# Kernel tuning notes

Measured on AMD Instinct MI355X. Metric: run time of the kernel, lower is better.

The kernel has to match this reference:

```python
import jax, jax.numpy as jnp
import numpy as np

N_NODES = 100000
N_EDGES = 1600000
NUM_GRAPHS = 64
D = 128      # num_node_features
H = 256      # hidden_dim
OUT = 1      # output_dim
GA = 6       # num_graph_attributes


def setup_inputs() -> dict:
    key = jax.random.key(0)
    ks = jax.random.split(key, 20)
    p = lambda k, shape: (jax.random.normal(k, shape, jnp.float32) * 0.02)
    return {
        "x": jax.random.normal(ks[0], (N_NODES, D), jnp.float32),
        "edge_index": jax.random.randint(ks[1], (2, N_EDGES), 0, N_NODES),
        "batch": jnp.sort(jax.random.randint(ks[2], (N_NODES,), 0, NUM_GRAPHS)),
        "graph_attr": jax.random.normal(ks[3], (NUM_GRAPHS, GA), jnp.float32),
        # conv1 MLP: Linear(D->H), ReLU, Linear(H->H)
        "w1a": p(ks[4], (D, H)), "b1a": p(ks[5], (H,)),
        "w1b": p(ks[6], (H, H)), "b1b": p(ks[7], (H,)),
        # conv2 MLP: Linear(H->H), ReLU, Linear(H->H)
        "w2a": p(ks[8], (H, H)), "b2a": p(ks[9], (H,)),
        "w2b": p(ks[10], (H, H)), "b2b": p(ks[11], (H,)),
        # head
        "wf1": p(ks[12], (H + GA, H)), "bf1": p(ks[13], (H,)),
        "wf2": p(ks[14], (H, OUT)), "bf2": p(ks[15], (OUT,)),
    }


def _gin_conv(x, src, dst, wa, ba, wb, bb):
    # GINConv with default eps=0: MLP((1+0)*x_i + sum_{j->i} x_j)
    agg = jax.ops.segment_sum(x[src], dst, num_segments=N_NODES)  # [N, d]
    h = x + agg
    h = jax.nn.relu(h @ wa + ba)
    return h @ wb + bb


def reference(x, edge_index, batch, graph_attr,
              w1a, b1a, w1b, b1b, w2a, b2a, w2b, b2b,
              wf1, bf1, wf2, bf2):
    src, dst = edge_index[0], edge_index[1]
    h = jax.nn.relu(_gin_conv(x, src, dst, w1a, b1a, w1b, b1b))  # [N, H]
    h = _gin_conv(h, src, dst, w2a, b2a, w2b, b2b)               # [N, H]
    # global mean pool per graph
    sums = jax.ops.segment_sum(h, batch, num_segments=NUM_GRAPHS)          # [G, H]
    cnts = jax.ops.segment_sum(jnp.ones((h.shape[0], 1), h.dtype), batch,
                               num_segments=NUM_GRAPHS)                    # [G, 1]
    pooled = sums / jnp.maximum(cnts, 1.0)
    g = jnp.concatenate([pooled, graph_attr.reshape(-1, GA)], axis=1)      # [G, H+GA]
    g = jax.nn.relu(g @ wf1 + bf1)
    return g @ wf2 + bf2                                                   # [G, OUT]
```

## Files before the change

kernel.cpp:

```cpp
#include <hip/hip_runtime.h>

#define N_NODES 100000
#define N_EDGES 1600000
#define NGRAPH  64
#define DIN     128
#define HID     256
#define GA      6

#define NBUCK  196
#define BSHIFT 9
#define BCAP   10240

typedef __attribute__((ext_vector_type(8))) short bf16x8;
typedef __attribute__((ext_vector_type(4))) float f32x4;

__device__ __forceinline__ unsigned short f2bf(float f) {
  unsigned int u = __float_as_uint(f);
  u += 0x7fffu + ((u >> 16) & 1u);
  return (unsigned short)(u >> 16);
}
__device__ __forceinline__ float bf_lo(unsigned int u) { return __uint_as_float(u << 16); }
__device__ __forceinline__ float bf_hi(unsigned int u) { return __uint_as_float(u & 0xffff0000u); }
__device__ __forceinline__ unsigned int packbf(float lo, float hi) {
  return (unsigned int)f2bf(lo) | ((unsigned int)f2bf(hi) << 16);
}

__device__ __forceinline__ void gload16(const void* g, void* l) {
  __builtin_amdgcn_global_load_lds(
      (const __attribute__((address_space(1))) unsigned int*)g,
      (__attribute__((address_space(3))) unsigned int*)l, 16, 0, 0);
}


__global__ __launch_bounds__(256) void cvt_all(const float* __restrict__ x,
                                               const float* __restrict__ w1a,
                                               const float* __restrict__ w1b,
                                               const float* __restrict__ w2a,
                                               const float* __restrict__ w2b,
                                               unsigned short* __restrict__ xo,
                                               unsigned short* __restrict__ o1a,
                                               unsigned short* __restrict__ o1b,
                                               unsigned short* __restrict__ o2a,
                                               unsigned short* __restrict__ o2b) {
  int bid = blockIdx.x, tid = threadIdx.x;
  if (bid < 12500) {
    size_t idx = ((size_t)bid * 256 + tid) * 4;
    float4 v = *(const float4*)&x[idx];
    ushort4 o;
    o.x = f2bf(v.x); o.y = f2bf(v.y); o.z = f2bf(v.z); o.w = f2bf(v.w);
    *(ushort4*)&xo[idx] = o;
    return;
  }
  bid -= 12500;
  const float* in; unsigned short* out; int shift, idx;
  if (bid < 128)      { in = w1a; out = o1a; shift = 7; idx = bid * 256 + tid; }
  else if (bid < 384) { in = w1b; out = o1b; shift = 8; idx = (bid - 128) * 256 + tid; }
  else if (bid < 640) { in = w2a; out = o2a; shift = 8; idx = (bid - 384) * 256 + tid; }
  else                { in = w2b; out = o2b; shift = 8; idx = (bid - 640) * 256 + tid; }
  int K = 1 << shift;
  int n = idx >> shift;
  int k = idx & (K - 1);
  out[idx] = f2bf(in[(size_t)k * HID + n]);
}


__global__ __launch_bounds__(256) void bin_kernel(const int* __restrict__ esrc,
                                                  const int* __restrict__ edst,
                                                  int* __restrict__ cursor,
                                                  unsigned int* __restrict__ tmp) {
  __shared__ unsigned int pk[4096];
  __shared__ unsigned char bkb[4096];
  __shared__ int hist[NBUCK], lbase[NBUCK + 1], gbase[NBUCK], lcur[NBUCK];
  const int tid = threadIdx.x;
  const int lane = tid & 63;
  const int ebase = blockIdx.x * 4096;
  const int n = min(4096, N_EDGES - ebase);
  if (tid < NBUCK) hist[tid] = 0;
  __syncthreads();
  unsigned int pkv[16]; int bk[16];
#pragma unroll
  for (int i = 0; i < 16; i++) {
    int e = ebase + i * 256 + tid;
    bk[i] = -1;
    if (e < N_EDGES) {
      int s = esrc[e], d = edst[e];
      bk[i] = d >> BSHIFT;
      pkv[i] = (unsigned int)s | ((unsigned int)(d & ((1 << BSHIFT) - 1)) << 17);
      atomicAdd(&hist[bk[i]], 1);
    }
  }
  __syncthreads();
  if (tid < 64) {
    int i0 = 4 * tid;
    int a0 = (i0 + 0 < NBUCK) ? hist[i0 + 0] : 0;
    int a1 = (i0 + 1 < NBUCK) ? hist[i0 + 1] : 0;
    int a2 = (i0 + 2 < NBUCK) ? hist[i0 + 2] : 0;
    int a3 = (i0 + 3 < NBUCK) ? hist[i0 + 3] : 0;
    int p = a0 + a1 + a2 + a3, sc = p;
#pragma unroll
    for (int off = 1; off < 64; off <<= 1) {
      int t = __shfl_up(sc, off);
      if (lane >= off) sc += t;
    }
    int excl = sc - p;
    if (i0 + 0 < NBUCK) lbase[i0 + 0] = excl;
    if (i0 + 1 < NBUCK) lbase[i0 + 1] = excl + a0;
    if (i0 + 2 < NBUCK) lbase[i0 + 2] = excl + a0 + a1;
    if (i0 + 3 < NBUCK) lbase[i0 + 3] = excl + a0 + a1 + a2;
    if (tid == 63) lbase[NBUCK] = sc;
  }
  __syncthreads();
  if (tid < NBUCK) {
    int c = hist[tid];
    gbase[tid] = c ? atomicAdd(&cursor[tid], c) : 0;
    lcur[tid] = lbase[tid];
  }
  __syncthreads();
#pragma unroll
  for (int i = 0; i < 16; i++) {
    if (bk[i] >= 0) {
      int pos = atomicAdd(&lcur[bk[i]], 1);
      pk[pos] = pkv[i];
      bkb[pos] = (unsigned char)bk[i];
    }
  }
  __syncthreads();
#pragma unroll
  for (int i = 0; i < 16; i++) {
    int idx = i * 256 + tid;
    if (idx < n) {
      int b = bkb[idx];
      tmp[(size_t)b * BCAP + gbase[b] + (idx - lbase[b])] = pk[idx];
    }
  }
}


__global__ __launch_bounds__(512) void sort_kernel(const unsigned int* __restrict__ tmp,
                                                   const int* __restrict__ cnt,
                                                   int* __restrict__ csr,
                                                   int* __restrict__ ssrc) {
  __shared__ int nhist[512], ncur[512];
  __shared__ int bb[NBUCK];
  __shared__ int wsum[8];
  const int b = blockIdx.x;
  const int tid = threadIdx.x;
  const int lane = tid & 63, wid = tid >> 6;
  if (tid < 64) {
    int i0 = 4 * tid;
    int a0 = (i0 + 0 < NBUCK) ? cnt[i0 + 0] : 0;
    int a1 = (i0 + 1 < NBUCK) ? cnt[i0 + 1] : 0;
    int a2 = (i0 + 2 < NBUCK) ? cnt[i0 + 2] : 0;
    int a3 = (i0 + 3 < NBUCK) ? cnt[i0 + 3] : 0;
    int p = a0 + a1 + a2 + a3, sc = p;
#pragma unroll
    for (int off = 1; off < 64; off <<= 1) {
      int t = __shfl_up(sc, off);
      if (lane >= off) sc += t;
    }
    int excl = sc - p;
    if (i0 + 0 < NBUCK) bb[i0 + 0] = excl;
    if (i0 + 1 < NBUCK) bb[i0 + 1] = excl + a0;
    if (i0 + 2 < NBUCK) bb[i0 + 2] = excl + a0 + a1;
    if (i0 + 3 < NBUCK) bb[i0 + 3] = excl + a0 + a1 + a2;
  }
  nhist[tid] = 0;
  __syncthreads();
  const int myCnt = cnt[b];
  const int ebase = bb[b];
  const unsigned int* srcp = tmp + (size_t)b * BCAP;
  for (int i = tid; i < myCnt; i += 512)
    atomicAdd(&nhist[srcp[i] >> 17], 1);
  __syncthreads();
  int v = nhist[tid];
  int sc = v;
#pragma unroll
  for (int off = 1; off < 64; off <<= 1) {
    int t = __shfl_up(sc, off);
    if (lane >= off) sc += t;
  }
  if (lane == 63) wsum[wid] = sc;
  __syncthreads();
  if (tid < 8) {
    int ws = wsum[tid];
#pragma unroll
    for (int off = 1; off < 8; off <<= 1) {
      int t = __shfl_up(ws, off);
      if (tid >= off) ws += t;
    }
    wsum[tid] = ws;
  }
  __syncthreads();
  int excl = ((wid > 0) ? wsum[wid - 1] : 0) + sc - v;
  ncur[tid] = excl;
  int node0 = (b << BSHIFT) + tid;
  if (node0 < N_NODES) csr[node0] = ebase + excl;
  if (b == 0 && tid == 0) csr[N_NODES] = N_EDGES;
  __syncthreads();
  for (int i = tid; i < myCnt; i += 512) {
    unsigned int pe = srcp[i];
    int pos = atomicAdd(&ncur[pe >> 17], 1);
    ssrc[ebase + pos] = (int)(pe & 0x1FFFF);
  }
}


__global__ __launch_bounds__(256) void agg1_kernel(const uint2* __restrict__ x,
                                                   const int* __restrict__ csr,
                                                   const int* __restrict__ ssrc,
                                                   uint2* __restrict__ out) {
  int node = blockIdx.x * 4 + (threadIdx.x >> 6);
  int lane = threadIdx.x & 63;
  int half = lane >> 5;
  int dl   = lane & 31;
  float a0 = 0.f, a1 = 0.f, a2 = 0.f, a3 = 0.f;
  if (half == 0) {
    uint2 u = x[(size_t)node * 32 + dl];
    a0 = bf_lo(u.x); a1 = bf_hi(u.x); a2 = bf_lo(u.y); a3 = bf_hi(u.y);
  }
  int s = csr[node], e = csr[node + 1];
  int i = s;
  for (; i + 8 <= e; i += 8) {
    int s0 = ssrc[i + half],     s1 = ssrc[i + 2 + half];
    int s2 = ssrc[i + 4 + half], s3 = ssrc[i + 6 + half];
    uint2 v0 = x[(size_t)s0 * 32 + dl];
    uint2 v1 = x[(size_t)s1 * 32 + dl];
    uint2 v2 = x[(size_t)s2 * 32 + dl];
    uint2 v3 = x[(size_t)s3 * 32 + dl];
    a0 += bf_lo(v0.x) + bf_lo(v1.x) + bf_lo(v2.x) + bf_lo(v3.x);
    a1 += bf_hi(v0.x) + bf_hi(v1.x) + bf_hi(v2.x) + bf_hi(v3.x);
    a2 += bf_lo(v0.y) + bf_lo(v1.y) + bf_lo(v2.y) + bf_lo(v3.y);
    a3 += bf_hi(v0.y) + bf_hi(v1.y) + bf_hi(v2.y) + bf_hi(v3.y);
  }
  for (; i + 2 <= e; i += 2) {
    int sn = ssrc[i + half];
    uint2 v = x[(size_t)sn * 32 + dl];
    a0 += bf_lo(v.x); a1 += bf_hi(v.x);
    a2 += bf_lo(v.y); a3 += bf_hi(v.y);
  }
  if (i < e && half == 0) {
    uint2 v = x[(size_t)ssrc[i] * 32 + dl];
    a0 += bf_lo(v.x); a1 += bf_hi(v.x);
    a2 += bf_lo(v.y); a3 += bf_hi(v.y);
  }
  a0 += __shfl_xor(a0, 32);
  a1 += __shfl_xor(a1, 32);
  a2 += __shfl_xor(a2, 32);
  a3 += __shfl_xor(a3, 32);
  if (half == 0) {
    uint2 o;
    o.x = packbf(a0, a1);
    o.y = packbf(a2, a3);
    out[(size_t)node * 32 + dl] = o;
  }
}

__global__ __launch_bounds__(256) void agg2_kernel(const uint2* __restrict__ x,
                                                   const int* __restrict__ csr,
                                                   const int* __restrict__ ssrc,
                                                   uint2* __restrict__ out) {
  int node = blockIdx.x * 4 + (threadIdx.x >> 6);
  int lane = threadIdx.x & 63;
  uint2 u = x[(size_t)node * 64 + lane];
  float a0 = bf_lo(u.x), a1 = bf_hi(u.x), a2 = bf_lo(u.y), a3 = bf_hi(u.y);
  int s = csr[node], e = csr[node + 1];
  int i = s;
  for (; i + 8 <= e; i += 8) {
    int n0 = ssrc[i],     n1 = ssrc[i + 1], n2 = ssrc[i + 2], n3 = ssrc[i + 3];
    int n4 = ssrc[i + 4], n5 = ssrc[i + 5], n6 = ssrc[i + 6], n7 = ssrc[i + 7];
    uint2 v0 = x[(size_t)n0 * 64 + lane];
    uint2 v1 = x[(size_t)n1 * 64 + lane];
    uint2 v2 = x[(size_t)n2 * 64 + lane];
    uint2 v3 = x[(size_t)n3 * 64 + lane];
    uint2 v4 = x[(size_t)n4 * 64 + lane];
    uint2 v5 = x[(size_t)n5 * 64 + lane];
    uint2 v6 = x[(size_t)n6 * 64 + lane];
    uint2 v7 = x[(size_t)n7 * 64 + lane];
    a0 += (bf_lo(v0.x) + bf_lo(v1.x)) + (bf_lo(v2.x) + bf_lo(v3.x)) +
          (bf_lo(v4.x) + bf_lo(v5.x)) + (bf_lo(v6.x) + bf_lo(v7.x));
    a1 += (bf_hi(v0.x) + bf_hi(v1.x)) + (bf_hi(v2.x) + bf_hi(v3.x)) +
          (bf_hi(v4.x) + bf_hi(v5.x)) + (bf_hi(v6.x) + bf_hi(v7.x));
    a2 += (bf_lo(v0.y) + bf_lo(v1.y)) + (bf_lo(v2.y) + bf_lo(v3.y)) +
          (bf_lo(v4.y) + bf_lo(v5.y)) + (bf_lo(v6.y) + bf_lo(v7.y));
    a3 += (bf_hi(v0.y) + bf_hi(v1.y)) + (bf_hi(v2.y) + bf_hi(v3.y)) +
          (bf_hi(v4.y) + bf_hi(v5.y)) + (bf_hi(v6.y) + bf_hi(v7.y));
  }
  for (; i < e; i++) {
    uint2 v = x[(size_t)ssrc[i] * 64 + lane];
    a0 += bf_lo(v.x); a1 += bf_hi(v.x);
    a2 += bf_lo(v.y); a3 += bf_hi(v.y);
  }
  uint2 o;
  o.x = packbf(a0, a1);
  o.y = packbf(a2, a3);
  out[(size_t)node * 64 + lane] = o;
}


template<int K, bool RELU>
__global__ __launch_bounds__(512)
void gemm128(const unsigned short* __restrict__ A,
             const unsigned short* __restrict__ Wt,
             const float* __restrict__ bias,
             unsigned short* __restrict__ C) {
  __shared__ unsigned short Asl[128 * 64];
  __shared__ unsigned short Wsl[256 * 64];
  const int tid = threadIdx.x;
  const int lane = tid & 63;
  const int w = tid >> 6;
  const int wm = w >> 2;
  const int wn = w & 3;
  const int l15 = lane & 15, l4 = lane >> 4, l7 = lane & 7;
  const int rowBase = blockIdx.x * 128;

  f32x4 acc[4][4] = {};

  for (int k0 = 0; k0 < K; k0 += 64) {
#pragma unroll
    for (int i = 0; i < 2; i++) {
      int c = i * 512 + tid;
      int m = c >> 3, koL = c & 7;
      int koS = koL ^ (m & 7);
      int gr = rowBase + m; if (gr >= N_NODES) gr = N_NODES - 1;
      gload16(&A[(size_t)gr * K + k0 + koS * 8], Asl + (size_t)c * 8);
    }
#pragma unroll
    for (int i = 0; i < 4; i++) {
      int c = i * 512 + tid;
      int n = c >> 3, koL = c & 7;
      int koS = koL ^ (n & 7);
      gload16(&Wt[(size_t)n * K + k0 + koS * 8], Wsl + (size_t)c * 8);
    }
    __syncthreads();
#pragma unroll
    for (int kk = 0; kk < 2; kk++) {
      int koX = (kk * 4 + l4) ^ l7;
      bf16x8 a[4], b[4];
#pragma unroll
      for (int f = 0; f < 4; f++) {
        int rowA = wm * 64 + f * 16 + l15;
        int rowB = wn * 64 + f * 16 + l15;
        a[f] = *(const bf16x8*)&Asl[(size_t)(rowA * 64 + koX * 8)];
        b[f] = *(const bf16x8*)&Wsl[(size_t)(rowB * 64 + koX * 8)];
      }
#pragma unroll
      for (int fm = 0; fm < 4; fm++)
#pragma unroll
        for (int fn = 0; fn < 4; fn++)
          acc[fm][fn] = __builtin_amdgcn_mfma_f32_16x16x32_bf16(a[fm], b[fn], acc[fm][fn], 0, 0, 0);
    }
    __syncthreads();
  }

#pragma unroll
  for (int fm = 0; fm < 4; fm++) {
    int r0 = rowBase + wm * 64 + fm * 16 + l4 * 4;
#pragma unroll
    for (int fn = 0; fn < 4; fn++) {
      int col = wn * 64 + fn * 16 + l15;
      float bb = bias[col];
#pragma unroll
      for (int j = 0; j < 4; j++) {
        int r = r0 + j;
        if (r < N_NODES) {
          float v = acc[fm][fn][j] + bb;
          if (RELU) v = fmaxf(v, 0.f);
          C[(size_t)r * HID + col] = f2bf(v);
        }
      }
    }
  }
}


__global__ __launch_bounds__(256) void pool_kernel(const unsigned short* __restrict__ H,
                                                   const int* __restrict__ batch,
                                                   float* __restrict__ sums,
                                                   float* __restrict__ cnts) {
  int d = threadIdx.x;
  int n0 = blockIdx.x * 128;
  int n1 = n0 + 128; if (n1 > N_NODES) n1 = N_NODES;
  int cur = batch[n0];
  float run = 0.f, runc = 0.f;
  for (int i = n0; i < n1; i++) {
    int b = batch[i];
    if (b != cur) {
      atomicAdd(&sums[(size_t)cur * HID + d], run);
      if (d == 0) atomicAdd(&cnts[cur], runc);
      run = 0.f; runc = 0.f; cur = b;
    }
    run += __uint_as_float(((unsigned int)H[(size_t)i * HID + d]) << 16);
    runc += 1.f;
  }
  atomicAdd(&sums[(size_t)cur * HID + d], run);
  if (d == 0) atomicAdd(&cnts[cur], runc);
}


__global__ __launch_bounds__(256) void head_kernel(const float* __restrict__ sums,
                                                   const float* __restrict__ cnts,
                                                   const float* __restrict__ gattr,
                                                   const float* __restrict__ wf1,
                                                   const float* __restrict__ bf1,
                                                   const float* __restrict__ wf2,
                                                   const float* __restrict__ bf2,
                                                   float* __restrict__ out) {
  int g = blockIdx.x, tid = threadIdx.x;
  __shared__ float gv[HID + GA + 2];
  __shared__ float red[256];
  float c = cnts[g]; c = fmaxf(c, 1.0f);
  gv[tid] = sums[(size_t)g * HID + tid] / c;
  if (tid < GA) gv[HID + tid] = gattr[g * GA + tid];
  if (tid < 2) gv[HID + GA + tid] = 0.f;
  __syncthreads();
  float ac0 = 0.f, ac1 = 0.f, ac2 = 0.f, ac3 = 0.f;
  float ac4 = 0.f, ac5 = 0.f, ac6 = 0.f, ac7 = 0.f;
  const float* wcol = wf1 + tid;
  int k = 0;
#pragma unroll 1
  for (; k + 8 <= HID + GA; k += 8) {
    float w0 = wcol[(size_t)(k + 0) * HID];
    float w1 = wcol[(size_t)(k + 1) * HID];
    float w2 = wcol[(size_t)(k + 2) * HID];
    float w3 = wcol[(size_t)(k + 3) * HID];
    float w4 = wcol[(size_t)(k + 4) * HID];
    float w5 = wcol[(size_t)(k + 5) * HID];
    float w6 = wcol[(size_t)(k + 6) * HID];
    float w7 = wcol[(size_t)(k + 7) * HID];
    ac0 = fmaf(gv[k + 0], w0, ac0);
    ac1 = fmaf(gv[k + 1], w1, ac1);
    ac2 = fmaf(gv[k + 2], w2, ac2);
    ac3 = fmaf(gv[k + 3], w3, ac3);
    ac4 = fmaf(gv[k + 4], w4, ac4);
    ac5 = fmaf(gv[k + 5], w5, ac5);
    ac6 = fmaf(gv[k + 6], w6, ac6);
    ac7 = fmaf(gv[k + 7], w7, ac7);
  }
  for (; k < HID + GA; k++)
    ac0 = fmaf(gv[k], wcol[(size_t)k * HID], ac0);
  float acc = ((ac0 + ac1) + (ac2 + ac3)) + ((ac4 + ac5) + (ac6 + ac7)) + bf1[tid];
  float h = fmaxf(acc, 0.f);
  red[tid] = h * wf2[tid];
  __syncthreads();
  for (int s = 128; s > 0; s >>= 1) {
    if (tid < s) red[tid] += red[tid + s];
    __syncthreads();
  }
  if (tid == 0) out[g] = red[0] + bf2[0];
}


extern "C" void kernel_launch(void* const* d_in, const int* in_sizes, int n_in,
                              void* d_out, int out_size, void* d_ws, size_t ws_size,
                              hipStream_t stream) {
  const float* x     = (const float*)d_in[0];
  const int*   eidx  = (const int*)d_in[1];
  const int*   batch = (const int*)d_in[2];
  const float* gattr = (const float*)d_in[3];
  const float* w1a = (const float*)d_in[4];  const float* b1a = (const float*)d_in[5];
  const float* w1b = (const float*)d_in[6];  const float* b1b = (const float*)d_in[7];
  const float* w2a = (const float*)d_in[8];  const float* b2a = (const float*)d_in[9];
  const float* w2b = (const float*)d_in[10]; const float* b2b = (const float*)d_in[11];
  const float* wf1 = (const float*)d_in[12]; const float* bf1 = (const float*)d_in[13];
  const float* wf2 = (const float*)d_in[14]; const float* bf2 = (const float*)d_in[15];
  float* out = (float*)d_out;

  const int* esrc = eidx;
  const int* edst = eidx + N_EDGES;

  char* w = (char*)d_ws;
  auto alloc = [&](size_t bytes) -> void* {
    void* p = (void*)w;
    w += (bytes + 255) & ~(size_t)255;
    return p;
  };
  unsigned short* B0 = (unsigned short*)alloc((size_t)N_NODES * DIN * 2);
  unsigned short* B1 = (unsigned short*)alloc((size_t)N_NODES * HID * 2);
  unsigned short* B2 = (unsigned short*)alloc((size_t)N_NODES * HID * 2);
  unsigned short* B3 = (unsigned short*)alloc((size_t)N_NODES * HID * 2);
  unsigned short* w1aT = (unsigned short*)alloc(256 * 128 * 2);
  unsigned short* w1bT = (unsigned short*)alloc(256 * 256 * 2);
  unsigned short* w2aT = (unsigned short*)alloc(256 * 256 * 2);
  unsigned short* w2bT = (unsigned short*)alloc(256 * 256 * 2);
  int*   csr    = (int*)alloc((N_NODES + 4) * 4);
  int*   cursor = (int*)alloc(NBUCK * 4);
  unsigned int* tmp = (unsigned int*)alloc((size_t)NBUCK * BCAP * 4);
  int*   ssrc   = (int*)alloc((size_t)N_EDGES * 4);
  float* sums   = (float*)alloc((size_t)NGRAPH * HID * 4);
  float* cnts   = (float*)alloc(NGRAPH * 4);

  hipMemsetAsync(cursor, 0, NBUCK * 4, stream);
  hipMemsetAsync(sums, 0, (size_t)NGRAPH * HID * 4 + 256, stream);

  cvt_all<<<12500 + 896, 256, 0, stream>>>(x, w1a, w1b, w2a, w2b,
                                           B0, w1aT, w1bT, w2aT, w2bT);

  bin_kernel<<<(N_EDGES + 4095) / 4096, 256, 0, stream>>>(esrc, edst, cursor, tmp);
  sort_kernel<<<NBUCK, 512, 0, stream>>>(tmp, cursor, csr, ssrc);

  const int ngemm = (N_NODES + 127) / 128;

  agg1_kernel<<<N_NODES / 4, 256, 0, stream>>>((const uint2*)B0, csr, ssrc, (uint2*)B1);
  gemm128<128, true><<<ngemm, 512, 0, stream>>>(B1, w1aT, b1a, B3);
  gemm128<256, true><<<ngemm, 512, 0, stream>>>(B3, w1bT, b1b, B2);
  agg2_kernel<<<N_NODES / 4, 256, 0, stream>>>((const uint2*)B2, csr, ssrc, (uint2*)B1);
  gemm128<256, true><<<ngemm, 512, 0, stream>>>(B1, w2aT, b2a, B3);
  gemm128<256, false><<<ngemm, 512, 0, stream>>>(B3, w2bT, b2b, B2);

  pool_kernel<<<(N_NODES + 127) / 128, 256, 0, stream>>>(B2, batch, sums, cnts);
  head_kernel<<<NGRAPH, 256, 0, stream>>>(sums, cnts, gattr, wf1, bf1, wf2, bf2, out);
}
```

Before: 411.5 us.

## Fuse global mean pooling into final GEMM epilogue and derive counts by binary search

The last GEMM no longer writes its 100k x 256 bf16 output. It reduces rows per graph in registers and shared memory, then atomically adds the partial sums into the pooled buffer, which removes the separate pool kernel and one full activation write and read. Node counts per graph are now computed in the head kernel by binary search over the sorted batch array, so the counts buffer goes away. The cost is extra shared-memory and global atomics in the GEMM epilogue, and the result now relies on batch being sorted. Pooling also sums fp32 values instead of bf16-rounded ones.

```diff
diff --git a/kernel.cpp b/kernel.cpp
--- a/kernel.cpp
+++ b/kernel.cpp
@@ -297,14 +297,19 @@
 }
 
 
-template<int K, bool RELU>
+#define GMAX 4
+
+template<int K, bool RELU, bool POOL>
 __global__ __launch_bounds__(512)
 void gemm128(const unsigned short* __restrict__ A,
              const unsigned short* __restrict__ Wt,
              const float* __restrict__ bias,
-             unsigned short* __restrict__ C) {
+             unsigned short* __restrict__ C,
+             const int* __restrict__ batch,
+             float* __restrict__ sums) {
   __shared__ unsigned short Asl[128 * 64];
   __shared__ unsigned short Wsl[256 * 64];
+  __shared__ float psum[POOL ? GMAX * HID : 1];
   const int tid = threadIdx.x;
   const int lane = tid & 63;
   const int w = tid >> 6;
@@ -313,6 +318,11 @@
   const int l15 = lane & 15, l4 = lane >> 4, l7 = lane & 7;
   const int rowBase = blockIdx.x * 128;
 
+  if (POOL) {
+#pragma unroll
+    for (int i = tid; i < GMAX * HID; i += 512) psum[i] = 0.f;
+  }
+
   f32x4 acc[4][4] = {};
 
   for (int k0 = 0; k0 < K; k0 += 64) {
@@ -352,53 +362,71 @@
     __syncthreads();
   }
 
-#pragma unroll
-  for (int fm = 0; fm < 4; fm++) {
-    int r0 = rowBase + wm * 64 + fm * 16 + l4 * 4;
+  if (!POOL) {
+#pragma unroll
+    for (int fm = 0; fm < 4; fm++) {
+      int r0 = rowBase + wm * 64 + fm * 16 + l4 * 4;
+#pragma unroll
+      for (int fn = 0; fn < 4; fn++) {
+        int col = wn * 64 + fn * 16 + l15;
+        float bb = bias[col];
+#pragma unroll
+        for (int j = 0; j < 4; j++) {
+          int r = r0 + j;
+          if (r < N_NODES) {
+            float v = acc[fm][fn][j] + bb;
+            if (RELU) v = fmaxf(v, 0.f);
+            C[(size_t)r * HID + col] = f2bf(v);
+          }
+        }
+      }
+    }
+  } else {
+    const int g0 = batch[rowBase];
 #pragma unroll
     for (int fn = 0; fn < 4; fn++) {
       int col = wn * 64 + fn * 16 + l15;
       float bb = bias[col];
-#pragma unroll
-      for (int j = 0; j < 4; j++) {
-        int r = r0 + j;
-        if (r < N_NODES) {
-          float v = acc[fm][fn][j] + bb;
-          if (RELU) v = fmaxf(v, 0.f);
-          C[(size_t)r * HID + col] = f2bf(v);
+      float part = 0.f;
+      int curgi = -1;
+#pragma unroll
+      for (int fm = 0; fm < 4; fm++) {
+#pragma unroll
+        for (int j = 0; j < 4; j++) {
+          int r = rowBase + wm * 64 + fm * 16 + l4 * 4 + j;
+          if (r < N_NODES) {
+            float v = acc[fm][fn][j] + bb;
+            int gi = batch[r] - g0;
+            if (gi != curgi) {
+              if (curgi >= 0) {
+                if (curgi < GMAX) atomicAdd(&psum[curgi * HID + col], part);
+                else atomicAdd(&sums[(size_t)(g0 + curgi) * HID + col], part);
+              }
+              curgi = gi; part = 0.f;
+            }
+            part += v;
+          }
         }
       }
-    }
-  }
-}
-
-
-__global__ __launch_bounds__(256) void pool_kernel(const unsigned short* __restrict__ H,
+      if (curgi >= 0) {
+        if (curgi < GMAX) atomicAdd(&psum[curgi * HID + col], part);
+        else atomicAdd(&sums[(size_t)(g0 + curgi) * HID + col], part);
+      }
+    }
+    __syncthreads();
+#pragma unroll
+    for (int i = tid; i < GMAX * HID; i += 512) {
+      float v = psum[i];
+      int g = g0 + (i >> 8);
+      if (v != 0.f && g < NGRAPH)
+        atomicAdd(&sums[(size_t)g * HID + (i & 255)], v);
+    }
+  }
+}
+
+
+__global__ __launch_bounds__(256) void head_kernel(const float* __restrict__ sums,
                                                    const int* __restrict__ batch,
-                                                   float* __restrict__ sums,
-                                                   float* __restrict__ cnts) {
-  int d = threadIdx.x;
-  int n0 = blockIdx.x * 128;
-  int n1 = n0 + 128; if (n1 > N_NODES) n1 = N_NODES;
-  int cur = batch[n0];
-  float run = 0.f, runc = 0.f;
-  for (int i = n0; i < n1; i++) {
-    int b = batch[i];
-    if (b != cur) {
-      atomicAdd(&sums[(size_t)cur * HID + d], run);
-      if (d == 0) atomicAdd(&cnts[cur], runc);
-      run = 0.f; runc = 0.f; cur = b;
-    }
-    run += __uint_as_float(((unsigned int)H[(size_t)i * HID + d]) << 16);
-    runc += 1.f;
-  }
-  atomicAdd(&sums[(size_t)cur * HID + d], run);
-  if (d == 0) atomicAdd(&cnts[cur], runc);
-}
-
-
-__global__ __launch_bounds__(256) void head_kernel(const float* __restrict__ sums,
-                                                   const float* __restrict__ cnts,
                                                    const float* __restrict__ gattr,
                                                    const float* __restrict__ wf1,
                                                    const float* __restrict__ bf1,
@@ -408,7 +436,16 @@
   int g = blockIdx.x, tid = threadIdx.x;
   __shared__ float gv[HID + GA + 2];
   __shared__ float red[256];
-  float c = cnts[g]; c = fmaxf(c, 1.0f);
+  auto lower_bound = [&](int key) {
+    int lo = 0, hi = N_NODES;
+    while (lo < hi) {
+      int mid = (lo + hi) >> 1;
+      if (batch[mid] < key) lo = mid + 1; else hi = mid;
+    }
+    return lo;
+  };
+  float c = (float)(lower_bound(g + 1) - lower_bound(g));
+  c = fmaxf(c, 1.0f);
   gv[tid] = sums[(size_t)g * HID + tid] / c;
   if (tid < GA) gv[HID + tid] = gattr[g * GA + tid];
   if (tid < 2) gv[HID + GA + tid] = 0.f;
@@ -487,10 +524,9 @@
   unsigned int* tmp = (unsigned int*)alloc((size_t)NBUCK * BCAP * 4);
   int*   ssrc   = (int*)alloc((size_t)N_EDGES * 4);
   float* sums   = (float*)alloc((size_t)NGRAPH * HID * 4);
-  float* cnts   = (float*)alloc(NGRAPH * 4);
 
   hipMemsetAsync(cursor, 0, NBUCK * 4, stream);
-  hipMemsetAsync(sums, 0, (size_t)NGRAPH * HID * 4 + 256, stream);
+  hipMemsetAsync(sums, 0, (size_t)NGRAPH * HID * 4, stream);
 
   cvt_all<<<12500 + 896, 256, 0, stream>>>(x, w1a, w1b, w2a, w2b,
                                            B0, w1aT, w1bT, w2aT, w2bT);
@@ -501,12 +537,11 @@
   const int ngemm = (N_NODES + 127) / 128;
 
   agg1_kernel<<<N_NODES / 4, 256, 0, stream>>>((const uint2*)B0, csr, ssrc, (uint2*)B1);
-  gemm128<128, true><<<ngemm, 512, 0, stream>>>(B1, w1aT, b1a, B3);
-  gemm128<256, true><<<ngemm, 512, 0, stream>>>(B3, w1bT, b1b, B2);
+  gemm128<128, true, false><<<ngemm, 512, 0, stream>>>(B1, w1aT, b1a, B3, nullptr, nullptr);
+  gemm128<256, true, false><<<ngemm, 512, 0, stream>>>(B3, w1bT, b1b, B2, nullptr, nullptr);
   agg2_kernel<<<N_NODES / 4, 256, 0, stream>>>((const uint2*)B2, csr, ssrc, (uint2*)B1);
-  gemm128<256, true><<<ngemm, 512, 0, stream>>>(B1, w2aT, b2a, B3);
-  gemm128<256, false><<<ngemm, 512, 0, stream>>>(B3, w2bT, b2b, B2);
-
-  pool_kernel<<<(N_NODES + 127) / 128, 256, 0, stream>>>(B2, batch, sums, cnts);
-  head_kernel<<<NGRAPH, 256, 0, stream>>>(sums, cnts, gattr, wf1, bf1, wf2, bf2, out);
-}
+  gemm128<256, true, false><<<ngemm, 512, 0, stream>>>(B1, w2aT, b2a, B3, nullptr, nullptr);
+  gemm128<256, false, true><<<ngemm, 512, 0, stream>>>(B3, w2bT, b2b, nullptr, batch, sums);
+
+  head_kernel<<<NGRAPH, 256, 0, stream>>>(sums, batch, gattr, wf1, bf1, wf2, bf2, out);
+}
```

Measured after the change: 403.6 us. Within noise of the previous version (-1.9%).
